# Kernel tuning notes

Hardware: AMD Instinct MI355X
Metric: run time of the kernel (lower is better)

## Reference

```python
import jax, jax.numpy as jnp
import numpy as np

B, N, DIN, DOUT, H = 4, 2048, 512, 512, 8
HD = DOUT // H


def setup_inputs() -> dict:
    key = jax.random.key(0)
    ks = jax.random.split(key, 8)
    x = jax.random.normal(ks[0], (B, N, DIN), dtype=jnp.float32)
    mask = jax.random.randint(ks[1], (B, 1, N, N), 0, 2, dtype=jnp.int32)
    s = 1.0 / np.sqrt(DIN)
    Wq = jax.random.uniform(ks[2], (DOUT, DIN), jnp.float32, -s, s)
    Wk = jax.random.uniform(ks[3], (DOUT, DIN), jnp.float32, -s, s)
    Wv = jax.random.uniform(ks[4], (DOUT, DIN), jnp.float32, -s, s)
    bq = jax.random.uniform(ks[5], (DOUT,), jnp.float32, -s, s)
    bk = jax.random.uniform(ks[6], (DOUT,), jnp.float32, -s, s)
    bv = jax.random.uniform(ks[7], (DOUT,), jnp.float32, -s, s)
    return {"x": x, "Wq": Wq, "bq": bq, "Wk": Wk, "bk": bk, "Wv": Wv, "bv": bv, "mask": mask}


def reference(x, Wq, bq, Wk, bk, Wv, bv, mask):
    b, n, _ = x.shape
    # torch Linear: y = x @ W.T + b ; split heads -> [b, h, n, hd]
    def proj(W, bias):
        y = jnp.einsum('bnd,od->bno', x, W) + bias
        return y.reshape(b, n, H, HD).transpose(0, 2, 1, 3)
    Q, K, V = proj(Wq, bq), proj(Wk, bk), proj(Wv, bv)
    scores = jnp.einsum('bhnd,bhmd->bhnm', Q, K) / np.sqrt(HD).astype(np.float32)
    scores = jnp.where(mask == 0, jnp.float32(-1e9), scores)
    attn = jax.nn.softmax(scores, axis=-1)
    ctx = jnp.einsum('bhnm,bhmd->bhnd', attn, V)
    ctx = ctx.transpose(0, 2, 1, 3).reshape(b, n, DOUT)
    return jax.nn.elu(ctx)
```

## Files before the change

### kernel.cpp

```cpp
#include <hip/hip_runtime.h>
#include <math.h>
#include <stdint.h>

#define CB 4
#define CN 2048
#define CDIN 512
#define CDOUT 512
#define CH 8
#define CHD 64
#define CM (CB * CN)
#define CBH (CB * CH)
#define NKT (CN / 64)

typedef _Float16 f16x8 __attribute__((ext_vector_type(8)));
typedef _Float16 f16x4 __attribute__((ext_vector_type(4)));
typedef float    f32x4 __attribute__((ext_vector_type(4)));

#define QSCALE 0.1803368801111204f

__device__ __forceinline__ void gl_lds16(const void* g, void* l) {
    __builtin_amdgcn_global_load_lds(
        (const __attribute__((address_space(1))) unsigned int*)g,
        (__attribute__((address_space(3))) unsigned int*)l, 16, 0, 0);
}


#define PB_X  2048
#define PB_WQ 2176
#define PB_WK 2304
#define PB_WV 2432
#define PB_MB 3456

__global__ __launch_bounds__(256) void prep_kernel(
    const float* __restrict__ x,  _Float16* __restrict__ xh,
    const float* __restrict__ Wq, _Float16* __restrict__ wqh,
    const float* __restrict__ Wk, _Float16* __restrict__ wkh,
    const float* __restrict__ Wv, _Float16* __restrict__ wvh,
    const int* __restrict__ mask, unsigned long long* __restrict__ mbits)
{
    const int bx = blockIdx.x;
    if (bx >= PB_WV) {
        const int lane = threadIdx.x & 63;
        const int Wi   = (bx - PB_WV) * 4 + (threadIdx.x >> 6);
        const int b    = Wi >> 10;
        const int t    = (Wi >> 5) & 31;
        const int n0   = (Wi & 31) * 64;
        unsigned long long myword = 0;
        #pragma unroll 8
        for (int it = 0; it < 64; ++it) {
            int v = mask[((size_t)(b * CN + n0 + it)) * CN + t * 64 + lane];
            unsigned long long bal = __ballot(v != 0);
            if (lane == it) myword = bal;
        }
        mbits[((size_t)(b * NKT + t)) * CN + n0 + lane] = myword;
        return;
    }
    const float* s; _Float16* d; int i;
    if (bx < PB_X)       { s = x;  d = xh;  i = bx * 2048 + threadIdx.x * 8; }
    else if (bx < PB_WQ) { s = Wq; d = wqh; i = (bx - PB_X)  * 2048 + threadIdx.x * 8; }
    else if (bx < PB_WK) { s = Wk; d = wkh; i = (bx - PB_WQ) * 2048 + threadIdx.x * 8; }
    else                 { s = Wv; d = wvh; i = (bx - PB_WK) * 2048 + threadIdx.x * 8; }
    float4 a = *(const float4*)&s[i];
    float4 b = *(const float4*)&s[i + 4];
    f16x8 h = {(_Float16)a.x, (_Float16)a.y, (_Float16)a.z, (_Float16)a.w,
               (_Float16)b.x, (_Float16)b.y, (_Float16)b.z, (_Float16)b.w};
    *(f16x8*)&d[i] = h;
}

__global__ __launch_bounds__(256) void proj_kernel(
    const _Float16* __restrict__ xh,
    const _Float16* __restrict__ Wqh, const float* __restrict__ bq,
    const _Float16* __restrict__ Wkh, const float* __restrict__ bk,
    const _Float16* __restrict__ Wvh, const float* __restrict__ bv,
    _Float16* __restrict__ Qf, _Float16* __restrict__ Kf, _Float16* __restrict__ Vt)
{
    const int z = blockIdx.z;
    const _Float16* Wp; const float* bias;
    if (z == 0)      { Wp = Wqh; bias = bq; }
    else if (z == 1) { Wp = Wkh; bias = bk; }
    else             { Wp = Wvh; bias = bv; }

    __shared__ _Float16 SM[18432];

    const int tid  = threadIdx.x;
    const int m0   = blockIdx.x * 128;
    const int o0   = blockIdx.y * 128;
    const int lane = tid & 63, w = tid >> 6;
    const int il   = lane & 15, quad = lane >> 4;
    const int rsub = lane >> 3;
    const int csw  = ((lane & 7) ^ (rsub & 7)) * 8;

    f32x4 acc[2][8] = {};

    for (int k0 = 0; k0 < CDIN; k0 += 64) {
        #pragma unroll
        for (int i = 0; i < 4; ++i) {
            const int r0 = w * 32 + i * 8;
            gl_lds16(&xh[(size_t)(m0 + r0 + rsub) * CDIN + k0 + csw], &SM[r0 * 64]);
            gl_lds16(&Wp[(size_t)(o0 + r0 + rsub) * CDIN + k0 + csw], &SM[8192 + r0 * 64]);
        }
        __syncthreads();

        #pragma unroll
        for (int dh = 0; dh < 2; ++dh) {
            const int ph = ((dh * 4 + quad) ^ (il & 7)) * 8;
            f16x8 X0 = *(const f16x8*)&SM[(w * 32 + il) * 64 + ph];
            f16x8 X1 = *(const f16x8*)&SM[(w * 32 + 16 + il) * 64 + ph];
            if (z < 2) {
                #pragma unroll
                for (int s = 0; s < 8; ++s) {
                    f16x8 Wv_ = *(const f16x8*)&SM[8192 + (s * 16 + il) * 64 + ph];
                    acc[0][s] = __builtin_amdgcn_mfma_f32_16x16x32_f16(Wv_, X0, acc[0][s], 0, 0, 0);
                    acc[1][s] = __builtin_amdgcn_mfma_f32_16x16x32_f16(Wv_, X1, acc[1][s], 0, 0, 0);
                }
            } else {
                #pragma unroll
                for (int s = 0; s < 8; ++s) {
                    f16x8 Wv_ = *(const f16x8*)&SM[8192 + (s * 16 + il) * 64 + ph];
                    acc[0][s] = __builtin_amdgcn_mfma_f32_16x16x32_f16(X0, Wv_, acc[0][s], 0, 0, 0);
                    acc[1][s] = __builtin_amdgcn_mfma_f32_16x16x32_f16(X1, Wv_, acc[1][s], 0, 0, 0);
                }
            }
        }
        __syncthreads();
    }

    const int b  = m0 / CN;
    const int nb = m0 & (CN - 1);
    if (z < 2) {
        const float sc = (z == 0) ? QSCALE : 1.0f;
        #pragma unroll
        for (int s = 0; s < 8; ++s) {
            #pragma unroll
            for (int mi = 0; mi < 2; ++mi) {
                f16x4 pv;
                #pragma unroll
                for (int r = 0; r < 4; ++r)
                    pv[r] = (_Float16)((acc[mi][s][r] + bias[o0 + s * 16 + quad * 4 + r]) * sc);
                *(f16x4*)&SM[(w * 32 + mi * 16 + il) * 140 + s * 16 + quad * 4] = pv;
            }
        }
    } else {
        #pragma unroll
        for (int s = 0; s < 8; ++s) {
            const float bval = bias[o0 + s * 16 + il];
            #pragma unroll
            for (int mi = 0; mi < 2; ++mi) {
                f16x4 pv = {(_Float16)(acc[mi][s][0] + bval),
                            (_Float16)(acc[mi][s][1] + bval),
                            (_Float16)(acc[mi][s][2] + bval),
                            (_Float16)(acc[mi][s][3] + bval)};
                *(f16x4*)&SM[(s * 16 + il) * 140 + w * 32 + mi * 16 + quad * 4] = pv;
            }
        }
    }
    __syncthreads();

    const int uu   = tid & 127;
    const int hseg = tid >> 7;
    const int bh   = b * CH + (o0 >> 6) + hseg;
    if (z < 2) {
        _Float16* dst = ((z == 0) ? Qf : Kf) + ((size_t)bh * CN + nb) * CHD;
        #pragma unroll
        for (int k = 0; k < 8; ++k) {
            int n = k * 16 + (uu >> 3);
            int d = (uu & 7) * 8;
            *(f16x8*)&dst[(size_t)n * CHD + d] =
                *(const f16x8*)&SM[n * 140 + hseg * 64 + d];
        }
    } else {
        _Float16* dst = Vt + (size_t)bh * CHD * CN + nb;
        #pragma unroll
        for (int k = 0; k < 8; ++k) {
            int d = k * 8 + (uu >> 4);
            int n = (uu & 15) * 8;
            *(f16x8*)&dst[(size_t)d * CN + n] =
                *(const f16x8*)&SM[(hseg * 64 + d) * 140 + n];
        }
    }
}

__global__ __launch_bounds__(512, 4) void attn_kernel(
    const _Float16* __restrict__ Qf, const _Float16* __restrict__ Kf,
    const _Float16* __restrict__ Vt, const unsigned long long* __restrict__ mbits,
    float* __restrict__ out)
{
    __shared__ _Float16 Ks[2][64 * 64];
    __shared__ _Float16 Vs[2][64 * 64];
    __shared__ _Float16 Ps[8][16 * 64];

    const int tid  = threadIdx.x;
    const int q0   = blockIdx.x * 128;
    const int bh   = blockIdx.y;
    const int b    = bh >> 3, h = bh & 7;
    const int lane = tid & 63, w = tid >> 6;
    const int il   = lane & 15, quad = lane >> 4;
    const int rsub = lane >> 3;
    const int csw  = ((lane & 7) ^ (rsub & 7)) * 8;

    const _Float16* Qb = Qf + (size_t)bh * CN * CHD;
    const _Float16* Kb = Kf + (size_t)bh * CN * CHD;
    const _Float16* Vb = Vt + (size_t)bh * CHD * CN;

    const int qg = q0 + w * 16 + il;
    const unsigned long long* mbb = mbits + (size_t)b * NKT * CN + qg;

    f16x8 Qa0 = *(const f16x8*)&Qb[(size_t)qg * CHD + quad * 8];
    f16x8 Qa1 = *(const f16x8*)&Qb[(size_t)qg * CHD + 32 + quad * 8];

    const f16x8 ones = {1.f16, 1.f16, 1.f16, 1.f16, 1.f16, 1.f16, 1.f16, 1.f16};

    const int phA0 = ((quad    ) ^ (il & 7)) * 8;
    const int phA1 = ((quad + 4) ^ (il & 7)) * 8;

    f32x4 oacc[4] = {};
    f32x4 lacc = {};

    gl_lds16(&Kb[(size_t)(w * 8 + rsub) * CHD + csw], &Ks[0][w * 8 * 64]);
    gl_lds16(&Vb[(size_t)(w * 8 + rsub) * CN + csw], &Vs[0][w * 8 * 64]);
    unsigned long long mn = mbb[0];
    __syncthreads();

    for (int kt = 0; kt < NKT; ++kt) {
        const int cur = kt & 1;
        const unsigned long long mcur = mn;

        if (kt < NKT - 1) {
            gl_lds16(&Kb[(size_t)((kt + 1) * 64 + w * 8 + rsub) * CHD + csw],
                     &Ks[cur ^ 1][w * 8 * 64]);
            gl_lds16(&Vb[(size_t)(w * 8 + rsub) * CN + (kt + 1) * 64 + csw],
                     &Vs[cur ^ 1][w * 8 * 64]);
            mn = mbb[(size_t)(kt + 1) * CN];
        }

        f32x4 st[4] = {};
        #pragma unroll
        for (int s = 0; s < 4; ++s) {
            f16x8 A0 = *(const f16x8*)&Ks[cur][(s * 16 + il) * 64 + phA0];
            f16x8 A1 = *(const f16x8*)&Ks[cur][(s * 16 + il) * 64 + phA1];
            st[s] = __builtin_amdgcn_mfma_f32_16x16x32_f16(A0, Qa0, st[s], 0, 0, 0);
            st[s] = __builtin_amdgcn_mfma_f32_16x16x32_f16(A1, Qa1, st[s], 0, 0, 0);
        }

        const uint32_t mlo = (uint32_t)mcur, mhi = (uint32_t)(mcur >> 32);
        #pragma unroll
        for (int s = 0; s < 4; ++s) {
            const uint32_t mm = (s < 2) ? mlo : mhi;
            const int base = (s & 1) * 16 + quad * 4;
            f16x4 pv;
            #pragma unroll
            for (int r = 0; r < 4; ++r) {
                float sv = ((mm >> (base + r)) & 1u) ? st[s][r] : -1e9f;
                pv[r] = (_Float16)__builtin_amdgcn_exp2f(sv);
            }
            *(f16x4*)&Ps[w][il * 64 +
                (((s * 2 + (quad >> 1)) ^ (il & 7)) << 3) + ((quad & 1) << 2)] = pv;
        }

        f16x8 Pa0 = *(const f16x8*)&Ps[w][il * 64 + phA0];
        f16x8 Pa1 = *(const f16x8*)&Ps[w][il * 64 + phA1];
        #pragma unroll
        for (int s = 0; s < 4; ++s) {
            f16x8 B0 = *(const f16x8*)&Vs[cur][(s * 16 + il) * 64 + phA0];
            f16x8 B1 = *(const f16x8*)&Vs[cur][(s * 16 + il) * 64 + phA1];
            oacc[s] = __builtin_amdgcn_mfma_f32_16x16x32_f16(Pa0, B0, oacc[s], 0, 0, 0);
            oacc[s] = __builtin_amdgcn_mfma_f32_16x16x32_f16(Pa1, B1, oacc[s], 0, 0, 0);
        }
        lacc = __builtin_amdgcn_mfma_f32_16x16x32_f16(Pa0, ones, lacc, 0, 0, 0);
        lacc = __builtin_amdgcn_mfma_f32_16x16x32_f16(Pa1, ones, lacc, 0, 0, 0);

        if (kt < NKT - 1) __syncthreads();
    }

    #pragma unroll
    for (int s = 0; s < 4; ++s) {
        const int d = h * CHD + s * 16 + il;
        #pragma unroll
        for (int r = 0; r < 4; ++r) {
            int n = q0 + w * 16 + quad * 4 + r;
            float c = oacc[s][r] / lacc[r];
            out[((size_t)b * CN + n) * CDOUT + d] = c > 0.f ? c : expm1f(c);
        }
    }
}

extern "C" void kernel_launch(void* const* d_in, const int* in_sizes, int n_in,
                              void* d_out, int out_size, void* d_ws, size_t ws_size,
                              hipStream_t stream) {
    const float* x    = (const float*)d_in[0];
    const float* Wq   = (const float*)d_in[1];
    const float* bq   = (const float*)d_in[2];
    const float* Wk   = (const float*)d_in[3];
    const float* bk   = (const float*)d_in[4];
    const float* Wv   = (const float*)d_in[5];
    const float* bv   = (const float*)d_in[6];
    const int*   mask = (const int*)d_in[7];
    float* out = (float*)d_out;

    const size_t nx = (size_t)CM * CDIN;
    const size_t nw = (size_t)CDOUT * CDIN;
    const size_t nt = (size_t)CBH * CN * CHD;
    _Float16* xh  = (_Float16*)d_ws;
    _Float16* wqh = xh + nx;
    _Float16* wkh = wqh + nw;
    _Float16* wvh = wkh + nw;
    _Float16* Qf  = wvh + nw;
    _Float16* Kf  = Qf + nt;
    _Float16* Vt  = Kf + nt;
    unsigned long long* mbits = (unsigned long long*)(Vt + nt);

    prep_kernel<<<dim3(PB_MB), 256, 0, stream>>>(
        x, xh, Wq, wqh, Wk, wkh, Wv, wvh, mask, mbits);
    proj_kernel<<<dim3(CM / 128, CDOUT / 128, 3), 256, 0, stream>>>(
        xh, wqh, bq, wkh, bk, wvh, bv, Qf, Kf, Vt);
    attn_kernel<<<dim3(CN / 128, CBH), 512, 0, stream>>>(
        Qf, Kf, Vt, mbits, out);
}
```

Before: 214.2 us.

## Move mask packing into projection grid and software-pipeline QK in attention

Mask bit-packing moves from the prep kernel into an extra z-slice of the projection kernel, so it runs alongside the GEMM blocks. The projection GEMM switches from global_load_lds to register-staged prefetch of the next K tile while the current tile is consumed. The attention loop becomes a software pipeline: QK^T for tile kt+1 is computed while tile kt's softmax and PV run, with a third V buffer and mask words prefetched two tiles ahead. This aims to hide load and MFMA latency, at the cost of more registers and LDS, which may reduce occupancy.

```diff
diff --git a/kernel.cpp b/kernel.cpp
--- a/kernel.cpp
+++ b/kernel.cpp
@@ -24,37 +24,18 @@
         (__attribute__((address_space(3))) unsigned int*)l, 16, 0, 0);
 }
 
-
 #define PB_X  2048
 #define PB_WQ 2176
 #define PB_WK 2304
 #define PB_WV 2432
-#define PB_MB 3456
 
 __global__ __launch_bounds__(256) void prep_kernel(
     const float* __restrict__ x,  _Float16* __restrict__ xh,
     const float* __restrict__ Wq, _Float16* __restrict__ wqh,
     const float* __restrict__ Wk, _Float16* __restrict__ wkh,
-    const float* __restrict__ Wv, _Float16* __restrict__ wvh,
-    const int* __restrict__ mask, unsigned long long* __restrict__ mbits)
+    const float* __restrict__ Wv, _Float16* __restrict__ wvh)
 {
     const int bx = blockIdx.x;
-    if (bx >= PB_WV) {
-        const int lane = threadIdx.x & 63;
-        const int Wi   = (bx - PB_WV) * 4 + (threadIdx.x >> 6);
-        const int b    = Wi >> 10;
-        const int t    = (Wi >> 5) & 31;
-        const int n0   = (Wi & 31) * 64;
-        unsigned long long myword = 0;
-        #pragma unroll 8
-        for (int it = 0; it < 64; ++it) {
-            int v = mask[((size_t)(b * CN + n0 + it)) * CN + t * 64 + lane];
-            unsigned long long bal = __ballot(v != 0);
-            if (lane == it) myword = bal;
-        }
-        mbits[((size_t)(b * NKT + t)) * CN + n0 + lane] = myword;
-        return;
-    }
     const float* s; _Float16* d; int i;
     if (bx < PB_X)       { s = x;  d = xh;  i = bx * 2048 + threadIdx.x * 8; }
     else if (bx < PB_WQ) { s = Wq; d = wqh; i = (bx - PB_X)  * 2048 + threadIdx.x * 8; }
@@ -72,9 +53,30 @@
     const _Float16* __restrict__ Wqh, const float* __restrict__ bq,
     const _Float16* __restrict__ Wkh, const float* __restrict__ bk,
     const _Float16* __restrict__ Wvh, const float* __restrict__ bv,
-    _Float16* __restrict__ Qf, _Float16* __restrict__ Kf, _Float16* __restrict__ Vt)
+    _Float16* __restrict__ Qf, _Float16* __restrict__ Kf, _Float16* __restrict__ Vt,
+    const int* __restrict__ mask, unsigned long long* __restrict__ mbits)
 {
     const int z = blockIdx.z;
+    const int tid = threadIdx.x;
+
+    if (z == 3) {
+        const int L = blockIdx.y * 64 + blockIdx.x;
+        const int lane = tid & 63, wv = tid >> 6;
+        for (int c = 0; c < 4; ++c) {
+            const int Wi = L * 16 + wv * 4 + c;
+            const int b = Wi >> 10, t = (Wi >> 5) & 31, n0 = (Wi & 31) * 64;
+            unsigned long long myword = 0;
+            #pragma unroll 8
+            for (int it = 0; it < 64; ++it) {
+                int v = mask[((size_t)(b * CN + n0 + it)) * CN + t * 64 + lane];
+                unsigned long long bal = __ballot(v != 0);
+                if (lane == it) myword = bal;
+            }
+            mbits[((size_t)(b * NKT + t)) * CN + n0 + lane] = myword;
+        }
+        return;
+    }
+
     const _Float16* Wp; const float* bias;
     if (z == 0)      { Wp = Wqh; bias = bq; }
     else if (z == 1) { Wp = Wkh; bias = bk; }
@@ -82,24 +84,38 @@
 
     __shared__ _Float16 SM[18432];
 
-    const int tid  = threadIdx.x;
     const int m0   = blockIdx.x * 128;
     const int o0   = blockIdx.y * 128;
     const int lane = tid & 63, w = tid >> 6;
     const int il   = lane & 15, quad = lane >> 4;
-    const int rsub = lane >> 3;
-    const int csw  = ((lane & 7) ^ (rsub & 7)) * 8;
+    const int srow = tid >> 3;
+    const int kc8  = tid & 7;
+    const int csw  = (kc8 ^ (srow & 7)) * 8;
 
     f32x4 acc[2][8] = {};
+    f16x8 xr[4], wr[4];
+
+    #pragma unroll
+    for (int i = 0; i < 4; ++i) {
+        xr[i] = *(const f16x8*)&xh[(size_t)(m0 + srow + i * 32) * CDIN + kc8 * 8];
+        wr[i] = *(const f16x8*)&Wp[(size_t)(o0 + srow + i * 32) * CDIN + kc8 * 8];
+    }
 
     for (int k0 = 0; k0 < CDIN; k0 += 64) {
         #pragma unroll
         for (int i = 0; i < 4; ++i) {
-            const int r0 = w * 32 + i * 8;
-            gl_lds16(&xh[(size_t)(m0 + r0 + rsub) * CDIN + k0 + csw], &SM[r0 * 64]);
-            gl_lds16(&Wp[(size_t)(o0 + r0 + rsub) * CDIN + k0 + csw], &SM[8192 + r0 * 64]);
+            *(f16x8*)&SM[(srow + i * 32) * 64 + csw] = xr[i];
+            *(f16x8*)&SM[8192 + (srow + i * 32) * 64 + csw] = wr[i];
         }
         __syncthreads();
+
+        if (k0 + 64 < CDIN) {
+            #pragma unroll
+            for (int i = 0; i < 4; ++i) {
+                xr[i] = *(const f16x8*)&xh[(size_t)(m0 + srow + i * 32) * CDIN + k0 + 64 + kc8 * 8];
+                wr[i] = *(const f16x8*)&Wp[(size_t)(o0 + srow + i * 32) * CDIN + k0 + 64 + kc8 * 8];
+            }
+        }
 
         #pragma unroll
         for (int dh = 0; dh < 2; ++dh) {
@@ -186,7 +202,7 @@
     float* __restrict__ out)
 {
     __shared__ _Float16 Ks[2][64 * 64];
-    __shared__ _Float16 Vs[2][64 * 64];
+    __shared__ _Float16 Vs[3][64 * 64];
     __shared__ _Float16 Ps[8][16 * 64];
 
     const int tid  = threadIdx.x;
@@ -196,7 +212,7 @@
     const int lane = tid & 63, w = tid >> 6;
     const int il   = lane & 15, quad = lane >> 4;
     const int rsub = lane >> 3;
-    const int csw  = ((lane & 7) ^ (rsub & 7)) * 8;
+    const int csw  = ((lane & 7) ^ rsub) * 8;
 
     const _Float16* Qb = Qf + (size_t)bh * CN * CHD;
     const _Float16* Kb = Kf + (size_t)bh * CN * CHD;
@@ -209,7 +225,6 @@
     f16x8 Qa1 = *(const f16x8*)&Qb[(size_t)qg * CHD + 32 + quad * 8];
 
     const f16x8 ones = {1.f16, 1.f16, 1.f16, 1.f16, 1.f16, 1.f16, 1.f16, 1.f16};
-
     const int phA0 = ((quad    ) ^ (il & 7)) * 8;
     const int phA1 = ((quad + 4) ^ (il & 7)) * 8;
 
@@ -218,31 +233,44 @@
 
     gl_lds16(&Kb[(size_t)(w * 8 + rsub) * CHD + csw], &Ks[0][w * 8 * 64]);
     gl_lds16(&Vb[(size_t)(w * 8 + rsub) * CN + csw], &Vs[0][w * 8 * 64]);
-    unsigned long long mn = mbb[0];
+    unsigned long long mk0 = mbb[0];
     __syncthreads();
+    gl_lds16(&Kb[(size_t)(64 + w * 8 + rsub) * CHD + csw], &Ks[1][w * 8 * 64]);
+    gl_lds16(&Vb[(size_t)(w * 8 + rsub) * CN + 64 + csw], &Vs[1][w * 8 * 64]);
+    unsigned long long mk1 = mbb[CN];
+
+    f32x4 st[4] = {};
+    #pragma unroll
+    for (int s = 0; s < 4; ++s) {
+        f16x8 A0 = *(const f16x8*)&Ks[0][(s * 16 + il) * 64 + phA0];
+        f16x8 A1 = *(const f16x8*)&Ks[0][(s * 16 + il) * 64 + phA1];
+        st[s] = __builtin_amdgcn_mfma_f32_16x16x32_f16(A0, Qa0, st[s], 0, 0, 0);
+        st[s] = __builtin_amdgcn_mfma_f32_16x16x32_f16(A1, Qa1, st[s], 0, 0, 0);
+    }
+    __syncthreads();
 
     for (int kt = 0; kt < NKT; ++kt) {
-        const int cur = kt & 1;
-        const unsigned long long mcur = mn;
-
-        if (kt < NKT - 1) {
-            gl_lds16(&Kb[(size_t)((kt + 1) * 64 + w * 8 + rsub) * CHD + csw],
-                     &Ks[cur ^ 1][w * 8 * 64]);
-            gl_lds16(&Vb[(size_t)(w * 8 + rsub) * CN + (kt + 1) * 64 + csw],
-                     &Vs[cur ^ 1][w * 8 * 64]);
-            mn = mbb[(size_t)(kt + 1) * CN];
-        }
-
-        f32x4 st[4] = {};
-        #pragma unroll
-        for (int s = 0; s < 4; ++s) {
-            f16x8 A0 = *(const f16x8*)&Ks[cur][(s * 16 + il) * 64 + phA0];
-            f16x8 A1 = *(const f16x8*)&Ks[cur][(s * 16 + il) * 64 + phA1];
-            st[s] = __builtin_amdgcn_mfma_f32_16x16x32_f16(A0, Qa0, st[s], 0, 0, 0);
-            st[s] = __builtin_amdgcn_mfma_f32_16x16x32_f16(A1, Qa1, st[s], 0, 0, 0);
-        }
-
-        const uint32_t mlo = (uint32_t)mcur, mhi = (uint32_t)(mcur >> 32);
+        unsigned long long mnew = 0;
+        if (kt + 2 < NKT) {
+            gl_lds16(&Kb[(size_t)((kt + 2) * 64 + w * 8 + rsub) * CHD + csw],
+                     &Ks[kt & 1][w * 8 * 64]);
+            gl_lds16(&Vb[(size_t)(w * 8 + rsub) * CN + (kt + 2) * 64 + csw],
+                     &Vs[(kt + 2) % 3][w * 8 * 64]);
+            mnew = mbb[(size_t)(kt + 2) * CN];
+        }
+
+        f32x4 stn[4] = {};
+        if (kt + 1 < NKT) {
+            #pragma unroll
+            for (int s = 0; s < 4; ++s) {
+                f16x8 A0 = *(const f16x8*)&Ks[(kt + 1) & 1][(s * 16 + il) * 64 + phA0];
+                f16x8 A1 = *(const f16x8*)&Ks[(kt + 1) & 1][(s * 16 + il) * 64 + phA1];
+                stn[s] = __builtin_amdgcn_mfma_f32_16x16x32_f16(A0, Qa0, stn[s], 0, 0, 0);
+                stn[s] = __builtin_amdgcn_mfma_f32_16x16x32_f16(A1, Qa1, stn[s], 0, 0, 0);
+            }
+        }
+
+        const uint32_t mlo = (uint32_t)mk0, mhi = (uint32_t)(mk0 >> 32);
         #pragma unroll
         for (int s = 0; s < 4; ++s) {
             const uint32_t mm = (s < 2) ? mlo : mhi;
@@ -261,15 +289,19 @@
         f16x8 Pa1 = *(const f16x8*)&Ps[w][il * 64 + phA1];
         #pragma unroll
         for (int s = 0; s < 4; ++s) {
-            f16x8 B0 = *(const f16x8*)&Vs[cur][(s * 16 + il) * 64 + phA0];
-            f16x8 B1 = *(const f16x8*)&Vs[cur][(s * 16 + il) * 64 + phA1];
+            f16x8 B0 = *(const f16x8*)&Vs[kt % 3][(s * 16 + il) * 64 + phA0];
+            f16x8 B1 = *(const f16x8*)&Vs[kt % 3][(s * 16 + il) * 64 + phA1];
             oacc[s] = __builtin_amdgcn_mfma_f32_16x16x32_f16(Pa0, B0, oacc[s], 0, 0, 0);
             oacc[s] = __builtin_amdgcn_mfma_f32_16x16x32_f16(Pa1, B1, oacc[s], 0, 0, 0);
         }
         lacc = __builtin_amdgcn_mfma_f32_16x16x32_f16(Pa0, ones, lacc, 0, 0, 0);
         lacc = __builtin_amdgcn_mfma_f32_16x16x32_f16(Pa1, ones, lacc, 0, 0, 0);
 
-        if (kt < NKT - 1) __syncthreads();
+        #pragma unroll
+        for (int s = 0; s < 4; ++s) st[s] = stn[s];
+        mk0 = mk1; mk1 = mnew;
+
+        if (kt + 1 < NKT) __syncthreads();
     }
 
     #pragma unroll
@@ -309,10 +341,10 @@
     _Float16* Vt  = Kf + nt;
     unsigned long long* mbits = (unsigned long long*)(Vt + nt);
 
-    prep_kernel<<<dim3(PB_MB), 256, 0, stream>>>(
-        x, xh, Wq, wqh, Wk, wkh, Wv, wvh, mask, mbits);
-    proj_kernel<<<dim3(CM / 128, CDOUT / 128, 3), 256, 0, stream>>>(
-        xh, wqh, bq, wkh, bk, wvh, bv, Qf, Kf, Vt);
+    prep_kernel<<<dim3(PB_WV), 256, 0, stream>>>(
+        x, xh, Wq, wqh, Wk, wkh, Wv, wvh);
+    proj_kernel<<<dim3(CM / 128, CDOUT / 128, 4), 256, 0, stream>>>(
+        xh, wqh, bq, wkh, bk, wvh, bv, Qf, Kf, Vt, mask, mbits);
     attn_kernel<<<dim3(CN / 128, CBH), 512, 0, stream>>>(
         Qf, Kf, Vt, mbits, out);
 }
```

Measured after the change: 214.4 us. About the same (+0.1%).
